# Kernel tuning notes

Measured on AMD Instinct MI355X. Metric: run time of the kernel, lower is better.

The kernel has to match this reference:

```python
import jax, jax.numpy as jnp
import numpy as np

D_MODEL = 1024
N_HEADS = 16
D_HEAD = D_MODEL // N_HEADS


def setup_inputs() -> dict:
    key = jax.random.key(0)
    ks = jax.random.split(key, 5)
    B, T = 2, 2048
    x = jax.random.normal(ks[0], (B, T, D_MODEL), dtype=jnp.float32)
    s = 1.0 / np.sqrt(D_MODEL)
    W_qkv = jax.random.normal(ks[1], (D_MODEL, 3 * D_MODEL), dtype=jnp.float32) * s
    b_qkv = jnp.zeros((3 * D_MODEL,), dtype=jnp.float32)
    W_proj = jax.random.normal(ks[2], (D_MODEL, D_MODEL), dtype=jnp.float32) * s
    b_proj = jnp.zeros((D_MODEL,), dtype=jnp.float32)
    return {"x": x, "W_qkv": W_qkv, "b_qkv": b_qkv, "W_proj": W_proj, "b_proj": b_proj}


def reference(x, W_qkv, b_qkv, W_proj, b_proj):
    B, T, C = x.shape
    qkv = x @ W_qkv + b_qkv                      # [B,T,3C]
    q, k, v = jnp.split(qkv, 3, axis=-1)
    # [B,T,C] -> [B,H,T,Dh]
    def to_heads(t):
        return t.reshape(B, T, N_HEADS, D_HEAD).transpose(0, 2, 1, 3)
    q, k, v = to_heads(q), to_heads(k), to_heads(v)
    scale = 1.0 / np.sqrt(D_HEAD).astype(np.float32)
    scores = jnp.einsum('bhqd,bhkd->bhqk', q, k) * scale  # [B,H,T,T]
    causal = jnp.tril(jnp.ones((T, T), dtype=bool))
    scores = jnp.where(causal, scores, -jnp.inf)
    attn = jax.nn.softmax(scores, axis=-1)
    out = jnp.einsum('bhqk,bhkd->bhqd', attn, v)          # [B,H,T,Dh]
    out = out.transpose(0, 2, 1, 3).reshape(B, T, C)
    return out @ W_proj + b_proj
```

## Files before the change

### kernel.cpp

```cpp
#include <hip/hip_runtime.h>
#include <hip/hip_bf16.h>
#include <cstdint>


using u16 = unsigned short;
using u32 = unsigned int;

typedef __bf16 bf16x8 __attribute__((ext_vector_type(8)));
typedef float f32x4 __attribute__((ext_vector_type(4)));

#define AS1 __attribute__((address_space(1)))
#define AS3 __attribute__((address_space(3)))

__device__ __forceinline__ u16 f2bf(float f) {
  u32 u = __float_as_uint(f);
  u += 0x7fffu + ((u >> 16) & 1u);
  return (u16)(u >> 16);
}
__device__ __forceinline__ u32 cvtpk(float a, float b) {
  u32 r;
  asm("v_cvt_pk_bf16_f32 %0, %1, %2" : "=v"(r) : "v"(a), "v"(b));
  return r;
}

__global__ __launch_bounds__(256) void prep(const float* __restrict__ x,
                                            u16* __restrict__ xb,
                                            const float* __restrict__ W0,
                                            u16* __restrict__ T0,
                                            const float* __restrict__ W1,
                                            u16* __restrict__ T1) {
  const int bx = blockIdx.x;
  const int tid = threadIdx.x;
  if (bx < 4096) {
    const int i = bx * 256 + tid;
    float4 v = ((const float4*)x)[i];
    ushort4 o;
    o.x = f2bf(v.x); o.y = f2bf(v.y); o.z = f2bf(v.z); o.w = f2bf(v.w);
    ((ushort4*)xb)[i] = o;
    return;
  }
  __shared__ float t[32][33];
  const int idx = bx - 4096;
  const int bxx = idx & 127, by = idx >> 7;
  const float* W; u16* Wt; int N, n0;
  if (bxx < 96) { W = W0; Wt = T0; N = 3072; n0 = bxx * 32; }
  else          { W = W1; Wt = T1; N = 1024; n0 = (bxx - 96) * 32; }
  const int k0 = by * 32;
  const int tx = tid & 31, ty = tid >> 5;
#pragma unroll
  for (int i = 0; i < 4; ++i)
    t[ty + i * 8][tx] = W[(size_t)(k0 + ty + i * 8) * N + n0 + tx];
  __syncthreads();
#pragma unroll
  for (int i = 0; i < 4; ++i)
    Wt[(size_t)(n0 + ty + i * 8) * 1024 + k0 + tx] = f2bf(t[tx][ty + i * 8]);
}

#define MFMA16 __builtin_amdgcn_mfma_f32_16x16x32_bf16

__global__ __launch_bounds__(256, 2) void gemm_qkv(const u16* __restrict__ A,
                                                   const u16* __restrict__ Bt,
                                                   const float* __restrict__ bias,
                                                   u16* __restrict__ qb,
                                                   u16* __restrict__ KF,
                                                   u16* __restrict__ VF,
                                                   float sc_val) {
  constexpr int NT = 16;
  constexpr int BUFO = 5 * 4096;
  __shared__ __align__(16) u16 sm[2 * BUFO];

  const int tid  = threadIdx.x;
  const int lane = tid & 63;
  const int w    = tid >> 6;
  const int quad = lane >> 4;
  const int l15  = lane & 15;

  const int bid = blockIdx.x;
  const int xcd = bid & 7, c = bid >> 3;
  const int mt = xcd * 4 + (c & 3);
  const int nt = c >> 2;
  const int bm = mt * 128, bn = nt * 192;

  const int wc = w * 48;

  const int srow = tid >> 3;
  const int scol = (((tid & 7) ^ ((tid >> 3) & 7)) << 3);

#define STAGEA(ch, ktile, bufo)                                                 \
  do {                                                                          \
    const u16* _s = A + (size_t)(bm + (ch) * 64 + srow) * 1024 +                \
                    ((ktile) << 6) + scol;                                      \
    u16* _d = sm + (bufo) + (ch) * 4096 + tid * 8;                              \
    __builtin_amdgcn_global_load_lds((AS1 const void*)_s, (AS3 void*)_d,        \
                                     16, 0, 0);                                 \
    __builtin_amdgcn_global_load_lds((AS1 const void*)(_s + (32 << 10)),        \
                                     (AS3 void*)(_d + 2048), 16, 0, 0);         \
  } while (0)
#define STAGEB(ch, ktile, bufo)                                                 \
  do {                                                                          \
    const u16* _s = Bt + (size_t)(bn + (ch) * 64 + srow) * 1024 +               \
                    ((ktile) << 6) + scol;                                      \
    u16* _d = sm + (bufo) + (2 + (ch)) * 4096 + tid * 8;                        \
    __builtin_amdgcn_global_load_lds((AS1 const void*)_s, (AS3 void*)_d,        \
                                     16, 0, 0);                                 \
    __builtin_amdgcn_global_load_lds((AS1 const void*)(_s + (32 << 10)),        \
                                     (AS3 void*)(_d + 2048), 16, 0, 0);         \
  } while (0)

  int abase_lo[4], abase_hi[4], bbase[3];
#pragma unroll
  for (int mi = 0; mi < 4; ++mi) {
    abase_lo[mi] = 0 * 4096 + (mi * 16 + l15) * 64;
    abase_hi[mi] = 1 * 4096 + (mi * 16 + l15) * 64;
  }
#pragma unroll
  for (int ni = 0; ni < 3; ++ni) {
    const int rb = wc + ni * 16 + l15;
    bbase[ni] = (2 + (rb >> 6)) * 4096 + (rb & 63) * 64;
  }
  const int sw0 = ((quad ^ (l15 & 7)) << 3);
  const int sw1 = sw0 ^ 32;

  STAGEA(0, 0, 0); STAGEA(1, 0, 0);
  STAGEB(0, 0, 0); STAGEB(1, 0, 0); STAGEB(2, 0, 0);
  STAGEA(0, 1, BUFO); STAGEA(1, 1, BUFO);
  asm volatile("s_waitcnt vmcnt(4)" ::: "memory");
  __builtin_amdgcn_s_barrier();

  f32x4 acc[8][3] = {};
  bf16x8 alo[4][2], ahi[4][2], b[3][2];

#pragma unroll 2
  for (int j = 0; j < NT; ++j) {
    const int bo  = (j & 1) * BUFO;
    const int nbo = bo ^ BUFO;
    const u16* smb = sm + bo;

#pragma unroll
    for (int mi = 0; mi < 4; ++mi) {
      alo[mi][0] = *(const bf16x8*)(smb + abase_lo[mi] + sw0);
      alo[mi][1] = *(const bf16x8*)(smb + abase_lo[mi] + sw1);
    }
#pragma unroll
    for (int ni = 0; ni < 2; ++ni) {
      b[ni][0] = *(const bf16x8*)(smb + bbase[ni] + sw0);
      b[ni][1] = *(const bf16x8*)(smb + bbase[ni] + sw1);
    }
#pragma unroll
    for (int mi = 0; mi < 4; ++mi) {
      ahi[mi][0] = *(const bf16x8*)(smb + abase_hi[mi] + sw0);
      ahi[mi][1] = *(const bf16x8*)(smb + abase_hi[mi] + sw1);
    }
    b[2][0] = *(const bf16x8*)(smb + bbase[2] + sw0);
    b[2][1] = *(const bf16x8*)(smb + bbase[2] + sw1);
    if (j + 1 < NT) { STAGEB(0, j + 1, nbo); STAGEB(1, j + 1, nbo); STAGEB(2, j + 1, nbo); }

    asm volatile("s_waitcnt lgkmcnt(10)" ::: "memory");
    __builtin_amdgcn_sched_barrier(0);
    __builtin_amdgcn_s_setprio(1);
#pragma unroll
    for (int mi = 0; mi < 4; ++mi)
#pragma unroll
      for (int ni = 0; ni < 2; ++ni) {
        acc[mi][ni] = MFMA16(alo[mi][0], b[ni][0], acc[mi][ni], 0, 0, 0);
        acc[mi][ni] = MFMA16(alo[mi][1], b[ni][1], acc[mi][ni], 0, 0, 0);
      }
    __builtin_amdgcn_s_setprio(0);
    asm volatile("s_waitcnt lgkmcnt(0)" ::: "memory");
    __builtin_amdgcn_sched_barrier(0);
    __builtin_amdgcn_s_barrier();
    if (j + 2 < NT) { STAGEA(0, j + 2, bo); STAGEA(1, j + 2, bo); }
    __builtin_amdgcn_s_setprio(1);
#pragma unroll
    for (int mi = 0; mi < 4; ++mi) {
      acc[mi][2] = MFMA16(alo[mi][0], b[2][0], acc[mi][2], 0, 0, 0);
      acc[mi][2] = MFMA16(alo[mi][1], b[2][1], acc[mi][2], 0, 0, 0);
      acc[4 + mi][0] = MFMA16(ahi[mi][0], b[0][0], acc[4 + mi][0], 0, 0, 0);
      acc[4 + mi][0] = MFMA16(ahi[mi][1], b[0][1], acc[4 + mi][0], 0, 0, 0);
    }
#pragma unroll
    for (int mi = 0; mi < 4; ++mi)
#pragma unroll
      for (int ni = 1; ni < 3; ++ni) {
        acc[4 + mi][ni] = MFMA16(ahi[mi][0], b[ni][0], acc[4 + mi][ni], 0, 0, 0);
        acc[4 + mi][ni] = MFMA16(ahi[mi][1], b[ni][1], acc[4 + mi][ni], 0, 0, 0);
      }
    __builtin_amdgcn_s_setprio(0);
    if (j + 2 < NT)
      asm volatile("s_waitcnt vmcnt(4)" ::: "memory");
    else
      asm volatile("s_waitcnt vmcnt(0)" ::: "memory");
    __builtin_amdgcn_s_barrier();
  }
#undef STAGEA
#undef STAGEB

  const int crow0 = bm + (quad << 2);
  const int ccol0 = bn + wc + l15;
#pragma unroll
  for (int ni = 0; ni < 3; ++ni) {
    const int n = ccol0 + ni * 16;
    const float bv = bias[n];
    if (n < 1024) {
#pragma unroll
      for (int mi = 0; mi < 8; ++mi) {
        const int m0 = crow0 + mi * 16;
#pragma unroll
        for (int r = 0; r < 4; ++r)
          qb[(size_t)(m0 + r) * 1024 + n] = f2bf((acc[mi][ni][r] + bv) * sc_val);
      }
    } else if (n < 2048) {
      const int hk = (n - 1024) >> 6;
      const int d  = (n - 1024) & 63;
      const int hh = d >> 5, qd = (d >> 3) & 3, jj = d & 7;
#pragma unroll
      for (int mi = 0; mi < 8; ++mi) {
#pragma unroll
        for (int r = 0; r < 4; ++r) {
          const int t  = crow0 + mi * 16 + r;
          const int bb = t >> 11, tt = t & 2047;
          const int kt = tt >> 6, mm = (tt >> 4) & 3, l = tt & 15;
          KF[((size_t)((bb * 16 + hk) * 32 + kt) * 8 + mm * 2 + hh) * 512 +
             (qd * 16 + l) * 8 + jj] = f2bf(acc[mi][ni][r] + bv);
        }
      }
    } else {
      const int hv = (n - 2048) >> 6;
      const int d  = (n - 2048) & 63;
      const int di = d >> 4, l = d & 15;
#pragma unroll
      for (int mi = 0; mi < 8; ++mi) {
#pragma unroll
        for (int r = 0; r < 4; ++r) {
          const int t  = crow0 + mi * 16 + r;
          const int bb = t >> 11, tt = t & 2047;
          const int kt = tt >> 6, to = tt & 63;
          const int mq = to >> 4, qd2 = (to >> 2) & 3, rr = to & 3;
          const int hh = mq >> 1, jj = (mq & 1) * 4 + rr;
          VF[((size_t)((bb * 16 + hv) * 32 + kt) * 8 + hh * 4 + di) * 512 +
             (qd2 * 16 + l) * 8 + jj] = f2bf(acc[mi][ni][r] + bv);
        }
      }
    }
  }
}

__global__ __launch_bounds__(256, 2) void gemm_proj(const u16* __restrict__ A,
                                                    const u16* __restrict__ Bt,
                                                    const float* __restrict__ bias,
                                                    float* __restrict__ C) {
  constexpr int NT = 16;
  constexpr int BUFO = 3 * 4096;
  __shared__ __align__(16) u16 sm[2 * BUFO];

  const int tid  = threadIdx.x;
  const int lane = tid & 63;
  const int w    = tid >> 6;
  const int quad = lane >> 4;
  const int l15  = lane & 15;

  const int bid = blockIdx.x;
  const int xcd = bid & 7, c = bid >> 3;
  const int mt = xcd * 4 + (c & 3);
  const int nt = c >> 2;
  const int bm = mt * 128, bn = nt * 64;

  const int wr = (w >> 1) * 64;
  const int wcC = (w & 1) * 32;

  const int srow = tid >> 3;
  const int scol = (((tid & 7) ^ ((tid >> 3) & 7)) << 3);

#define PSTAGEA(ch, ktile, bufo)                                                \
  do {                                                                          \
    const u16* _s = A + (size_t)(bm + (ch) * 64 + srow) * 1024 +                \
                    ((ktile) << 6) + scol;                                      \
    u16* _d = sm + (bufo) + (ch) * 4096 + tid * 8;                              \
    __builtin_amdgcn_global_load_lds((AS1 const void*)_s, (AS3 void*)_d,        \
                                     16, 0, 0);                                 \
    __builtin_amdgcn_global_load_lds((AS1 const void*)(_s + (32 << 10)),        \
                                     (AS3 void*)(_d + 2048), 16, 0, 0);         \
  } while (0)
#define PSTAGEB(ktile, bufo)                                                    \
  do {                                                                          \
    const u16* _s = Bt + (size_t)(bn + srow) * 1024 + ((ktile) << 6) + scol;    \
    u16* _d = sm + (bufo) + 2 * 4096 + tid * 8;                                 \
    __builtin_amdgcn_global_load_lds((AS1 const void*)_s, (AS3 void*)_d,        \
                                     16, 0, 0);                                 \
    __builtin_amdgcn_global_load_lds((AS1 const void*)(_s + (32 << 10)),        \
                                     (AS3 void*)(_d + 2048), 16, 0, 0);         \
  } while (0)

  int abase[4], bbase[2];
#pragma unroll
  for (int mi = 0; mi < 4; ++mi)
    abase[mi] = (w >> 1) * 4096 + (mi * 16 + l15) * 64;
#pragma unroll
  for (int ni = 0; ni < 2; ++ni)
    bbase[ni] = 2 * 4096 + (wcC + ni * 16 + l15) * 64;
  const int sw0 = ((quad ^ (l15 & 7)) << 3);
  const int sw1 = sw0 ^ 32;

  PSTAGEA(0, 0, 0); PSTAGEA(1, 0, 0); PSTAGEB(0, 0);
  PSTAGEA(0, 1, BUFO); PSTAGEA(1, 1, BUFO);
  asm volatile("s_waitcnt vmcnt(4)" ::: "memory");
  __builtin_amdgcn_s_barrier();

  f32x4 acc[4][2] = {};
  bf16x8 a[4][2], b[2][2];

#pragma unroll 2
  for (int j = 0; j < NT; ++j) {
    const int bo  = (j & 1) * BUFO;
    const int nbo = bo ^ BUFO;
    const u16* smb = sm + bo;

#pragma unroll
    for (int mi = 0; mi < 4; ++mi) {
      a[mi][0] = *(const bf16x8*)(smb + abase[mi] + sw0);
      a[mi][1] = *(const bf16x8*)(smb + abase[mi] + sw1);
    }
#pragma unroll
    for (int ni = 0; ni < 2; ++ni) {
      b[ni][0] = *(const bf16x8*)(smb + bbase[ni] + sw0);
      b[ni][1] = *(const bf16x8*)(smb + bbase[ni] + sw1);
    }
    if (j + 1 < NT) PSTAGEB(j + 1, nbo);

    asm volatile("s_waitcnt lgkmcnt(2)" ::: "memory");
    __builtin_amdgcn_sched_barrier(0);
    __builtin_amdgcn_s_setprio(1);
#pragma unroll
    for (int mi = 0; mi < 4; ++mi) {
      acc[mi][0] = MFMA16(a[mi][0], b[0][0], acc[mi][0], 0, 0, 0);
      acc[mi][0] = MFMA16(a[mi][1], b[0][1], acc[mi][0], 0, 0, 0);
    }
    __builtin_amdgcn_s_setprio(0);
    asm volatile("s_waitcnt lgkmcnt(0)" ::: "memory");
    __builtin_amdgcn_sched_barrier(0);
    __builtin_amdgcn_s_barrier();
    if (j + 2 < NT) { PSTAGEA(0, j + 2, bo); PSTAGEA(1, j + 2, bo); }
    __builtin_amdgcn_s_setprio(1);
#pragma unroll
    for (int mi = 0; mi < 4; ++mi) {
      acc[mi][1] = MFMA16(a[mi][0], b[1][0], acc[mi][1], 0, 0, 0);
      acc[mi][1] = MFMA16(a[mi][1], b[1][1], acc[mi][1], 0, 0, 0);
    }
    __builtin_amdgcn_s_setprio(0);
    if (j + 2 < NT)
      asm volatile("s_waitcnt vmcnt(4)" ::: "memory");
    else
      asm volatile("s_waitcnt vmcnt(0)" ::: "memory");
    __builtin_amdgcn_s_barrier();
  }
#undef PSTAGEA
#undef PSTAGEB

  const int crow0 = bm + wr + (quad << 2);
  const int ccol0 = bn + wcC + l15;
#pragma unroll
  for (int ni = 0; ni < 2; ++ni) {
    const int n = ccol0 + ni * 16;
    const float bv = bias[n];
#pragma unroll
    for (int mi = 0; mi < 4; ++mi) {
      const int m0 = crow0 + mi * 16;
#pragma unroll
      for (int r = 0; r < 4; ++r)
        C[(size_t)(m0 + r) * 1024 + n] = acc[mi][ni][r] + bv;
    }
  }
}

__global__ __launch_bounds__(128, 2) void attn_bal(const u16* __restrict__ qb,
                                                   const u16* __restrict__ KF,
                                                   const u16* __restrict__ VF,
                                                   u16* __restrict__ out) {
  const int bid = blockIdx.x;
  const int c   = bid >> 3;
  const int u   = c & 31;
  const int bh  = (bid & 7) | ((c >> 5) << 3);
  const int b = bh >> 4, h = bh & 15;
  const int tid = threadIdx.x;
  const int lane = tid & 63;
  const int par  = tid >> 6;
  const int quad = lane >> 4;
  const int l15  = lane & 15;

  __shared__ float CB[64][41];

  const u16* qbase = qb + (size_t)b * 2048 * 1024 + h * 64;
  const size_t fb = (size_t)bh * 32 * 4096 + lane * 8;
  const u16* kfb = KF + fb;
  const u16* vfb = VF + fb;

  union { u32 u4[4]; bf16x8 v; } onesu;
  onesu.u4[0] = onesu.u4[1] = onesu.u4[2] = onesu.u4[3] = 0x3f803f80u;
  const bf16x8 onesf = onesu.v;

  u16* const outb = out + (size_t)b * 2048 * 1024 + h * 64 + l15;

  auto run_group = [&](int g32) {
    const int q0 = g32 * 32;
    const int ktmax = g32 >> 1;

    bf16x8 qf[2][2];
#pragma unroll
    for (int g = 0; g < 2; ++g)
#pragma unroll
      for (int hh = 0; hh < 2; ++hh)
        qf[g][hh] = *(const bf16x8*)(qbase + (size_t)(q0 + g * 16 + l15) * 1024 +
                                     hh * 32 + quad * 8);

    f32x4 accO[2][4] = {};
    f32x4 accL[2] = {};

    bf16x8 kA[4][2], kB[4][2], vA[2][4], vB[2][4];
    {
      const u16* kp = kfb + (size_t)par * 4096;
      const u16* vp = vfb + (size_t)par * 4096;
#pragma unroll
      for (int m = 0; m < 4; ++m)
#pragma unroll
        for (int hh = 0; hh < 2; ++hh)
          kA[m][hh] = *(const bf16x8*)(kp + (m * 2 + hh) * 512);
#pragma unroll
      for (int hh = 0; hh < 2; ++hh)
#pragma unroll
        for (int di = 0; di < 4; ++di)
          vA[hh][di] = *(const bf16x8*)(vp + (hh * 4 + di) * 512);
    }

    auto tile = [&](int kt, bf16x8 (&KC)[4][2], bf16x8 (&KN)[4][2],
                    bf16x8 (&VC)[2][4], bf16x8 (&VN)[2][4]) {
      const int ktn = (kt + 2 <= ktmax) ? kt + 2 : ktmax;
      const u16* kpn = kfb + (size_t)ktn * 4096;
      const u16* vpn = vfb + (size_t)ktn * 4096;
#pragma unroll
      for (int m = 0; m < 4; ++m)
#pragma unroll
        for (int hh = 0; hh < 2; ++hh)
          KN[m][hh] = *(const bf16x8*)(kpn + (m * 2 + hh) * 512);
#pragma unroll
      for (int hh = 0; hh < 2; ++hh)
#pragma unroll
        for (int di = 0; di < 4; ++di)
          VN[hh][di] = *(const bf16x8*)(vpn + (hh * 4 + di) * 512);

      const bool diag = (kt == ktmax);
      bf16x8 ap[2][2];
#pragma unroll
      for (int g = 0; g < 2; ++g) {
        f32x4 sT[4] = {};
#pragma unroll
        for (int m = 0; m < 4; ++m) {
          sT[m] = MFMA16(KC[m][0], qf[g][0], sT[m], 0, 0, 0);
          sT[m] = MFMA16(KC[m][1], qf[g][1], sT[m], 0, 0, 0);
        }
        float pv[4][4];
        if (diag) {
          const int qgl = q0 + g * 16 + l15;
#pragma unroll
          for (int m = 0; m < 4; ++m)
#pragma unroll
            for (int r = 0; r < 4; ++r) {
              const bool msk = (kt * 64 + m * 16 + quad * 4 + r) > qgl;
              pv[m][r] = msk ? 0.f : __builtin_amdgcn_exp2f(sT[m][r]);
            }
        } else {
#pragma unroll
          for (int m = 0; m < 4; ++m)
#pragma unroll
            for (int r = 0; r < 4; ++r)
              pv[m][r] = __builtin_amdgcn_exp2f(sT[m][r]);
        }
        union { u32 u4[4]; bf16x8 v; } t0, t1;
        t0.u4[0] = cvtpk(pv[0][0], pv[0][1]);
        t0.u4[1] = cvtpk(pv[0][2], pv[0][3]);
        t0.u4[2] = cvtpk(pv[1][0], pv[1][1]);
        t0.u4[3] = cvtpk(pv[1][2], pv[1][3]);
        t1.u4[0] = cvtpk(pv[2][0], pv[2][1]);
        t1.u4[1] = cvtpk(pv[2][2], pv[2][3]);
        t1.u4[2] = cvtpk(pv[3][0], pv[3][1]);
        t1.u4[3] = cvtpk(pv[3][2], pv[3][3]);
        ap[g][0] = t0.v;
        ap[g][1] = t1.v;
      }

#pragma unroll
      for (int hh = 0; hh < 2; ++hh)
#pragma unroll
        for (int di = 0; di < 4; ++di) {
          bf16x8 bv = VC[hh][di];
#pragma unroll
          for (int g = 0; g < 2; ++g)
            accO[g][di] = MFMA16(ap[g][hh], bv, accO[g][di], 0, 0, 0);
        }
#pragma unroll
      for (int g = 0; g < 2; ++g) {
        accL[g] = MFMA16(ap[g][0], onesf, accL[g], 0, 0, 0);
        accL[g] = MFMA16(ap[g][1], onesf, accL[g], 0, 0, 0);
      }
    };

    for (int kt = par; kt <= ktmax; ) {
      tile(kt, kA, kB, vA, vB); kt += 2;
      if (kt > ktmax) break;
      tile(kt, kB, kA, vB, vA); kt += 2;
    }

    if (par) {
      float* cb = CB[lane];
#pragma unroll
      for (int g = 0; g < 2; ++g) {
#pragma unroll
        for (int di = 0; di < 4; ++di)
#pragma unroll
          for (int r = 0; r < 4; ++r)
            cb[g * 16 + di * 4 + r] = accO[g][di][r];
#pragma unroll
        for (int r = 0; r < 4; ++r)
          cb[32 + g * 4 + r] = accL[g][r];
      }
    }
    __syncthreads();
    if (!par) {
      const float* cb = CB[lane];
#pragma unroll
      for (int g = 0; g < 2; ++g) {
#pragma unroll
        for (int di = 0; di < 4; ++di)
#pragma unroll
          for (int r = 0; r < 4; ++r)
            accO[g][di][r] += cb[g * 16 + di * 4 + r];
#pragma unroll
        for (int r = 0; r < 4; ++r)
          accL[g][r] += cb[32 + g * 4 + r];
      }
#pragma unroll
      for (int g = 0; g < 2; ++g)
#pragma unroll
        for (int r = 0; r < 4; ++r) {
          const float inv = 1.f / accL[g][r];
          const int q = q0 + g * 16 + quad * 4 + r;
          u16* op = outb + (size_t)q * 1024;
#pragma unroll
          for (int di = 0; di < 4; ++di)
            op[di * 16] = f2bf(accO[g][di][r] * inv);
        }
    }
    __syncthreads();
  };

  run_group(63 - u);
  run_group(u);
}

extern "C" void kernel_launch(void* const* d_in, const int* in_sizes, int n_in,
                              void* d_out, int out_size, void* d_ws, size_t ws_size,
                              hipStream_t stream) {
  const float* x     = (const float*)d_in[0];
  const float* Wqkv  = (const float*)d_in[1];
  const float* bqkv  = (const float*)d_in[2];
  const float* Wproj = (const float*)d_in[3];
  const float* bproj = (const float*)d_in[4];
  float* out = (float*)d_out;

  char* ws = (char*)d_ws;
  u16* xb     = (u16*)(ws);
  u16* wqkvT  = (u16*)(ws + 8388608);
  u16* wprojT = (u16*)(ws + 14680064);
  u16* qb     = (u16*)(ws + 16777216);
  u16* KF     = (u16*)(ws + 25165824);
  u16* VF     = (u16*)(ws + 33554432);
  u16* att    = (u16*)(ws + 41943040);

  constexpr float cs = 0.18033688011f;

  prep<<<8192, 256, 0, stream>>>(x, xb, Wqkv, wqkvT, Wproj, wprojT);

  gemm_qkv<<<dim3(512), 256, 0, stream>>>(xb, wqkvT, bqkv, qb, KF, VF, cs);

  attn_bal<<<dim3(1024), 128, 0, stream>>>(qb, KF, VF, att);

  gemm_proj<<<dim3(512), 256, 0, stream>>>(att, wprojT, bproj, out);
}
```

Before: 149.6 us.

## Widen weight transpose tiles, retile QKV GEMM warps 2x2, vectorize V stores

The weight-transpose prep now uses 32x128 tiles with float4 loads and 16-byte packed bf16 stores, which cuts the block count and moves from scalar to vector global accesses. The QKV GEMM changes its per-warp tile from 128x48 to a 2x2 warp grid of 64x96. That lowers the LDS fragment reads per MFMA and reorders the MFMA schedule, with the lgkmcnt wait adjusted to match. The V scatter in the epilogue now packs four rows into one 8-byte store using v_cvt_pk_bf16_f32. The cost is more live B fragments and a different register footprint under the 2-waves-per-SIMD launch bound.

```diff
diff --git a/kernel.cpp b/kernel.cpp
--- a/kernel.cpp
+++ b/kernel.cpp
@@ -39,21 +39,36 @@
     ((ushort4*)xb)[i] = o;
     return;
   }
-  __shared__ float t[32][33];
+  __shared__ float t[32][129];
   const int idx = bx - 4096;
-  const int bxx = idx & 127, by = idx >> 7;
+  const int nti = idx & 31, kti = idx >> 5;
   const float* W; u16* Wt; int N, n0;
-  if (bxx < 96) { W = W0; Wt = T0; N = 3072; n0 = bxx * 32; }
-  else          { W = W1; Wt = T1; N = 1024; n0 = (bxx - 96) * 32; }
-  const int k0 = by * 32;
-  const int tx = tid & 31, ty = tid >> 5;
-#pragma unroll
-  for (int i = 0; i < 4; ++i)
-    t[ty + i * 8][tx] = W[(size_t)(k0 + ty + i * 8) * N + n0 + tx];
+  if (nti < 24) { W = W0; Wt = T0; N = 3072; n0 = nti * 128; }
+  else          { W = W1; Wt = T1; N = 1024; n0 = (nti - 24) * 128; }
+  const int k0 = kti * 32;
+
+  const int kr = tid >> 5, nc = (tid & 31) * 4;
+#pragma unroll
+  for (int i = 0; i < 4; ++i) {
+    const float4 v = *(const float4*)&W[(size_t)(k0 + kr + i * 8) * N + n0 + nc];
+    t[kr + i * 8][nc + 0] = v.x;
+    t[kr + i * 8][nc + 1] = v.y;
+    t[kr + i * 8][nc + 2] = v.z;
+    t[kr + i * 8][nc + 3] = v.w;
+  }
   __syncthreads();
-#pragma unroll
-  for (int i = 0; i < 4; ++i)
-    Wt[(size_t)(n0 + ty + i * 8) * 1024 + k0 + tx] = f2bf(t[tx][ty + i * 8]);
+  const int r = tid >> 1, kc = (tid & 1) * 16;
+#pragma unroll
+  for (int h = 0; h < 2; ++h) {
+    union { u32 w[4]; uint4 v; } o;
+#pragma unroll
+    for (int jj = 0; jj < 4; ++jj) {
+      const u16 lo = f2bf(t[kc + h * 8 + jj * 2 + 0][r]);
+      const u16 hi = f2bf(t[kc + h * 8 + jj * 2 + 1][r]);
+      o.w[jj] = (u32)lo | ((u32)hi << 16);
+    }
+    *(uint4*)&Wt[(size_t)(n0 + r) * 1024 + k0 + kc + h * 8] = o.v;
+  }
 }
 
 #define MFMA16 __builtin_amdgcn_mfma_f32_16x16x32_bf16
@@ -81,7 +96,8 @@
   const int nt = c >> 2;
   const int bm = mt * 128, bn = nt * 192;
 
-  const int wc = w * 48;
+  const int wr = (w >> 1) * 64;
+  const int wc = (w & 1) * 96;
 
   const int srow = tid >> 3;
   const int scol = (((tid & 7) ^ ((tid >> 3) & 7)) << 3);
@@ -107,14 +123,12 @@
                                      (AS3 void*)(_d + 2048), 16, 0, 0);         \
   } while (0)
 
-  int abase_lo[4], abase_hi[4], bbase[3];
-#pragma unroll
-  for (int mi = 0; mi < 4; ++mi) {
-    abase_lo[mi] = 0 * 4096 + (mi * 16 + l15) * 64;
-    abase_hi[mi] = 1 * 4096 + (mi * 16 + l15) * 64;
-  }
-#pragma unroll
-  for (int ni = 0; ni < 3; ++ni) {
+  int abase[4], bbase[6];
+#pragma unroll
+  for (int mi = 0; mi < 4; ++mi)
+    abase[mi] = (wr >> 6) * 4096 + (mi * 16 + l15) * 64;
+#pragma unroll
+  for (int ni = 0; ni < 6; ++ni) {
     const int rb = wc + ni * 16 + l15;
     bbase[ni] = (2 + (rb >> 6)) * 4096 + (rb & 63) * 64;
   }
@@ -127,8 +141,8 @@
   asm volatile("s_waitcnt vmcnt(4)" ::: "memory");
   __builtin_amdgcn_s_barrier();
 
-  f32x4 acc[8][3] = {};
-  bf16x8 alo[4][2], ahi[4][2], b[3][2];
+  f32x4 acc[4][6] = {};
+  bf16x8 a[4][2], b[6][2];
 
 #pragma unroll 2
   for (int j = 0; j < NT; ++j) {
@@ -138,8 +152,8 @@
 
 #pragma unroll
     for (int mi = 0; mi < 4; ++mi) {
-      alo[mi][0] = *(const bf16x8*)(smb + abase_lo[mi] + sw0);
-      alo[mi][1] = *(const bf16x8*)(smb + abase_lo[mi] + sw1);
+      a[mi][0] = *(const bf16x8*)(smb + abase[mi] + sw0);
+      a[mi][1] = *(const bf16x8*)(smb + abase[mi] + sw1);
     }
 #pragma unroll
     for (int ni = 0; ni < 2; ++ni) {
@@ -147,23 +161,21 @@
       b[ni][1] = *(const bf16x8*)(smb + bbase[ni] + sw1);
     }
 #pragma unroll
-    for (int mi = 0; mi < 4; ++mi) {
-      ahi[mi][0] = *(const bf16x8*)(smb + abase_hi[mi] + sw0);
-      ahi[mi][1] = *(const bf16x8*)(smb + abase_hi[mi] + sw1);
-    }
-    b[2][0] = *(const bf16x8*)(smb + bbase[2] + sw0);
-    b[2][1] = *(const bf16x8*)(smb + bbase[2] + sw1);
+    for (int ni = 2; ni < 6; ++ni) {
+      b[ni][0] = *(const bf16x8*)(smb + bbase[ni] + sw0);
+      b[ni][1] = *(const bf16x8*)(smb + bbase[ni] + sw1);
+    }
     if (j + 1 < NT) { STAGEB(0, j + 1, nbo); STAGEB(1, j + 1, nbo); STAGEB(2, j + 1, nbo); }
 
-    asm volatile("s_waitcnt lgkmcnt(10)" ::: "memory");
+    asm volatile("s_waitcnt lgkmcnt(8)" ::: "memory");
     __builtin_amdgcn_sched_barrier(0);
     __builtin_amdgcn_s_setprio(1);
 #pragma unroll
     for (int mi = 0; mi < 4; ++mi)
 #pragma unroll
       for (int ni = 0; ni < 2; ++ni) {
-        acc[mi][ni] = MFMA16(alo[mi][0], b[ni][0], acc[mi][ni], 0, 0, 0);
-        acc[mi][ni] = MFMA16(alo[mi][1], b[ni][1], acc[mi][ni], 0, 0, 0);
+        acc[mi][ni] = MFMA16(a[mi][0], b[ni][0], acc[mi][ni], 0, 0, 0);
+        acc[mi][ni] = MFMA16(a[mi][1], b[ni][1], acc[mi][ni], 0, 0, 0);
       }
     __builtin_amdgcn_s_setprio(0);
     asm volatile("s_waitcnt lgkmcnt(0)" ::: "memory");
@@ -172,18 +184,11 @@
     if (j + 2 < NT) { STAGEA(0, j + 2, bo); STAGEA(1, j + 2, bo); }
     __builtin_amdgcn_s_setprio(1);
 #pragma unroll
-    for (int mi = 0; mi < 4; ++mi) {
-      acc[mi][2] = MFMA16(alo[mi][0], b[2][0], acc[mi][2], 0, 0, 0);
-      acc[mi][2] = MFMA16(alo[mi][1], b[2][1], acc[mi][2], 0, 0, 0);
-      acc[4 + mi][0] = MFMA16(ahi[mi][0], b[0][0], acc[4 + mi][0], 0, 0, 0);
-      acc[4 + mi][0] = MFMA16(ahi[mi][1], b[0][1], acc[4 + mi][0], 0, 0, 0);
-    }
-#pragma unroll
     for (int mi = 0; mi < 4; ++mi)
 #pragma unroll
-      for (int ni = 1; ni < 3; ++ni) {
-        acc[4 + mi][ni] = MFMA16(ahi[mi][0], b[ni][0], acc[4 + mi][ni], 0, 0, 0);
-        acc[4 + mi][ni] = MFMA16(ahi[mi][1], b[ni][1], acc[4 + mi][ni], 0, 0, 0);
+      for (int ni = 2; ni < 6; ++ni) {
+        acc[mi][ni] = MFMA16(a[mi][0], b[ni][0], acc[mi][ni], 0, 0, 0);
+        acc[mi][ni] = MFMA16(a[mi][1], b[ni][1], acc[mi][ni], 0, 0, 0);
       }
     __builtin_amdgcn_s_setprio(0);
     if (j + 2 < NT)
@@ -195,15 +200,15 @@
 #undef STAGEA
 #undef STAGEB
 
-  const int crow0 = bm + (quad << 2);
+  const int crow0 = bm + wr + (quad << 2);
   const int ccol0 = bn + wc + l15;
 #pragma unroll
-  for (int ni = 0; ni < 3; ++ni) {
+  for (int ni = 0; ni < 6; ++ni) {
     const int n = ccol0 + ni * 16;
     const float bv = bias[n];
     if (n < 1024) {
 #pragma unroll
-      for (int mi = 0; mi < 8; ++mi) {
+      for (int mi = 0; mi < 4; ++mi) {
         const int m0 = crow0 + mi * 16;
 #pragma unroll
         for (int r = 0; r < 4; ++r)
@@ -214,7 +219,7 @@
       const int d  = (n - 1024) & 63;
       const int hh = d >> 5, qd = (d >> 3) & 3, jj = d & 7;
 #pragma unroll
-      for (int mi = 0; mi < 8; ++mi) {
+      for (int mi = 0; mi < 4; ++mi) {
 #pragma unroll
         for (int r = 0; r < 4; ++r) {
           const int t  = crow0 + mi * 16 + r;
@@ -229,17 +234,17 @@
       const int d  = (n - 2048) & 63;
       const int di = d >> 4, l = d & 15;
 #pragma unroll
-      for (int mi = 0; mi < 8; ++mi) {
-#pragma unroll
-        for (int r = 0; r < 4; ++r) {
-          const int t  = crow0 + mi * 16 + r;
-          const int bb = t >> 11, tt = t & 2047;
-          const int kt = tt >> 6, to = tt & 63;
-          const int mq = to >> 4, qd2 = (to >> 2) & 3, rr = to & 3;
-          const int hh = mq >> 1, jj = (mq & 1) * 4 + rr;
-          VF[((size_t)((bb * 16 + hv) * 32 + kt) * 8 + hh * 4 + di) * 512 +
-             (qd2 * 16 + l) * 8 + jj] = f2bf(acc[mi][ni][r] + bv);
-        }
+      for (int mi = 0; mi < 4; ++mi) {
+        const int t  = crow0 + mi * 16;
+        const int bb = t >> 11, tt = t & 2047;
+        const int kt = tt >> 6, to = tt & 63;
+        const int mq = to >> 4, qd2 = (to >> 2) & 3;
+        const int hh = mq >> 1, jj = (mq & 1) * 4;
+        uint2 o;
+        o.x = cvtpk(acc[mi][ni][0] + bv, acc[mi][ni][1] + bv);
+        o.y = cvtpk(acc[mi][ni][2] + bv, acc[mi][ni][3] + bv);
+        *(uint2*)&VF[((size_t)((bb * 16 + hv) * 32 + kt) * 8 + hh * 4 + di) * 512 +
+                     (qd2 * 16 + l) * 8 + jj] = o;
       }
     }
   }
@@ -577,7 +582,7 @@
 
   constexpr float cs = 0.18033688011f;
 
-  prep<<<8192, 256, 0, stream>>>(x, xb, Wqkv, wqkvT, Wproj, wprojT);
+  prep<<<5120, 256, 0, stream>>>(x, xb, Wqkv, wqkvT, Wproj, wprojT);
 
   gemm_qkv<<<dim3(512), 256, 0, stream>>>(xb, wqkvT, bqkv, qb, KF, VF, cs);
 
```

Result: slower. 154.7 us (+3.4%).
